# Performance work log

Measured on AMD Instinct MI355X. Metric: run time of the kernel, lower is better.

## Reference

```python
import jax, jax.numpy as jnp
import numpy as np

# Surrogate spike: forward heaviside, backward 1/(1+5|x|)^2
@jax.custom_vjp
def spike_fn(x):
    return (x >= 0).astype(x.dtype)

def _spike_fwd(x):
    return (x >= 0).astype(x.dtype), x

def _spike_bwd(x, g):
    return (g / (1.0 + 5.0 * jnp.abs(x)) ** 2,)

spike_fn.defvjp(_spike_fwd, _spike_bwd)

B, T, C, H, TDA, NCLS = 512, 1000, 64, 128, 150, 4
EPS = 1e-5


def setup_inputs() -> dict:
    key = jax.random.key(0)
    ks = jax.random.split(key, 16)
    inp = {}
    inp['kin_spikes_seq'] = jax.random.uniform(ks[0], (B, T, C), dtype=jnp.float32)
    inp['tda_features'] = jax.random.normal(ks[1], (B, TDA), dtype=jnp.float32)
    # spike_fc: init normal(mean=0.02, std=0.1), zero bias
    inp['W_fc'] = 0.02 + 0.1 * jax.random.normal(ks[2], (H, C), dtype=jnp.float32)
    inp['b_fc'] = jnp.zeros((H,), jnp.float32)
    # tda_net
    inp['W_t1'] = 0.08 * jax.random.normal(ks[3], (64, TDA), dtype=jnp.float32)
    inp['b_t1'] = jnp.zeros((64,), jnp.float32)
    inp['W_t2'] = 0.12 * jax.random.normal(ks[4], (64, 64), dtype=jnp.float32)
    inp['b_t2'] = jnp.zeros((64,), jnp.float32)
    # classifier: Linear(H+64 -> 128), BN(128), Linear(128 -> NCLS)
    inp['W_c1'] = 0.07 * jax.random.normal(ks[5], (128, H + 64), dtype=jnp.float32)
    inp['b_c1'] = jnp.zeros((128,), jnp.float32)
    inp['bn_gamma'] = jnp.ones((128,), jnp.float32)
    inp['bn_beta'] = jnp.zeros((128,), jnp.float32)
    inp['W_c2'] = 0.09 * jax.random.normal(ks[6], (NCLS, 128), dtype=jnp.float32)
    inp['b_c2'] = jnp.zeros((NCLS,), jnp.float32)
    return inp


def reference(kin_spikes_seq, tda_features, W_fc, b_fc, W_t1, b_t1, W_t2, b_t2,
              W_c1, b_c1, bn_gamma, bn_beta, W_c2, b_c2):
    Bsz, Tlen, _ = kin_spikes_seq.shape
    Hd = W_fc.shape[0]
    # Precompute all per-step input currents with one big GEMM (same math as
    # per-step Linear, since weights are time-invariant).
    currents = jnp.einsum('btc,hc->bth', kin_spikes_seq, W_fc) + b_fc  # [B,T,H]
    cur_t_first = jnp.transpose(currents, (1, 0, 2))  # [T,B,H]

    def step(carry, cur):
        mem, counts = carry
        mem = 0.9 * mem + cur
        spk = spike_fn(mem - 1.0)
        mem = mem * (1.0 - spk)
        return (mem, counts + spk), None

    init = (jnp.zeros((Bsz, Hd), kin_spikes_seq.dtype),
            jnp.zeros((Bsz, Hd), kin_spikes_seq.dtype))
    (mem, spike_counts), _ = jax.lax.scan(step, init, cur_t_first)

    firing_rate = spike_counts / Tlen
    tda_h = jax.nn.relu(tda_features @ W_t1.T + b_t1)
    tda_out = jax.nn.relu(tda_h @ W_t2.T + b_t2)
    fused = jnp.concatenate([firing_rate, tda_out], axis=1)  # [B, H+64]

    h = fused @ W_c1.T + b_c1
    # BatchNorm1d (training-mode batch statistics, biased variance)
    mean = jnp.mean(h, axis=0)
    var = jnp.var(h, axis=0)
    h = (h - mean) * jax.lax.rsqrt(var + EPS) * bn_gamma + bn_beta
    h = jax.nn.relu(h)  # dropout is identity in eval
    out = h @ W_c2.T + b_c2
    return out, spike_counts
```

## Files before the change

### kernel.cpp

```cpp
#include <hip/hip_runtime.h>
#include <stdint.h>

#define BB 512
#define TT 1000
#define CC 64
#define HH 128
#define TDA_F 150
#define NCLS 4
#define EPSV 1e-5f
#define NSEG 8
#define SEGLEN 125
#define WARM 51

typedef _Float16 half8 __attribute__((ext_vector_type(8)));
typedef float floatx4 __attribute__((ext_vector_type(4)));

__device__ __forceinline__ void split8(const float* v, half8& hi, half8& lo) {
#pragma unroll
  for (int i = 0; i < 8; ++i) {
    _Float16 h = (_Float16)v[i];
    hi[i] = h;
    lo[i] = (_Float16)(v[i] - (float)h);
  }
}

__global__ __launch_bounds__(64, 2) void snn_scan(
    const float* __restrict__ kin, const float* __restrict__ Wfc,
    const float* __restrict__ bfc, float* __restrict__ part)
{
  const int lane = threadIdx.x;
  const int q = lane >> 4;
  const int m = lane & 15;
  const int b = blockIdx.x >> 3;
  const int seg = blockIdx.x & 7;

  const int t0 = (seg == 0) ? 0 : SEGLEN * seg - WARM;
  const int ntiles = (seg == 0) ? 8 : 11;
  const int lo = SEGLEN * seg;
  const int hi = lo + SEGLEN;

  half8 bh[8][2], bl[8][2];
  float bv[8];
#pragma unroll
  for (int ht = 0; ht < 8; ++ht) {
    bv[ht] = bfc[ht * 16 + m];
#pragma unroll
    for (int kh = 0; kh < 2; ++kh) {
      const float* wp = Wfc + (ht * 16 + m) * CC + kh * 32 + q * 8;
      float av[8];
      float4 w0 = *(const float4*)(wp);
      float4 w1 = *(const float4*)(wp + 4);
      av[0] = w0.x; av[1] = w0.y; av[2] = w0.z; av[3] = w0.w;
      av[4] = w1.x; av[5] = w1.y; av[6] = w1.z; av[7] = w1.w;
      split8(av, bh[ht][kh], bl[ht][kh]);
    }
  }

  __shared__ float cur[16][132];

  const float* ab = kin + ((size_t)b * TT + (t0 + m)) * CC + q * 8;

  float4 p0 = *(const float4*)(ab);
  float4 p1 = *(const float4*)(ab + 4);
  float4 p2 = *(const float4*)(ab + 32);
  float4 p3 = *(const float4*)(ab + 36);

  float mem0 = 0.f, mem1 = 0.f, cnt0 = 0.f, cnt1 = 0.f;

  for (int tile = 0; tile < ntiles; ++tile) {
    float4 c0 = p0, c1 = p1, c2 = p2, c3 = p3;
    if (tile + 1 < ntiles) {
      ab += 16 * CC;
      p0 = *(const float4*)(ab);
      p1 = *(const float4*)(ab + 4);
      p2 = *(const float4*)(ab + 32);
      p3 = *(const float4*)(ab + 36);
    }

    float av0[8] = {c0.x, c0.y, c0.z, c0.w, c1.x, c1.y, c1.z, c1.w};
    float av1[8] = {c2.x, c2.y, c2.z, c2.w, c3.x, c3.y, c3.z, c3.w};
    half8 ah0, al0, ah1, al1;
    split8(av0, ah0, al0);
    split8(av1, ah1, al1);

#pragma unroll
    for (int ht = 0; ht < 8; ++ht) {
      floatx4 acc = {bv[ht], bv[ht], bv[ht], bv[ht]};
      acc = __builtin_amdgcn_mfma_f32_16x16x32_f16(al0, bh[ht][0], acc, 0, 0, 0);
      acc = __builtin_amdgcn_mfma_f32_16x16x32_f16(ah0, bl[ht][0], acc, 0, 0, 0);
      acc = __builtin_amdgcn_mfma_f32_16x16x32_f16(ah0, bh[ht][0], acc, 0, 0, 0);
      acc = __builtin_amdgcn_mfma_f32_16x16x32_f16(al1, bh[ht][1], acc, 0, 0, 0);
      acc = __builtin_amdgcn_mfma_f32_16x16x32_f16(ah1, bl[ht][1], acc, 0, 0, 0);
      acc = __builtin_amdgcn_mfma_f32_16x16x32_f16(ah1, bh[ht][1], acc, 0, 0, 0);
#pragma unroll
      for (int r = 0; r < 4; ++r) cur[q * 4 + r][ht * 16 + m] = acc[r];
    }

    const int tb = t0 + tile * 16;
#pragma unroll
    for (int s = 0; s < 16; ++s) {
      const float cu0 = cur[s][lane];
      const float cu1 = cur[s][lane + 64];
      const int t = tb + s;
      const bool act = (t >= lo) && (t < hi);
      mem0 = fmaf(0.9f, mem0, cu0);
      mem1 = fmaf(0.9f, mem1, cu1);
      const bool s0 = (mem0 >= 1.0f);
      const bool s1 = (mem1 >= 1.0f);
      cnt0 += (act && s0) ? 1.0f : 0.0f;
      cnt1 += (act && s1) ? 1.0f : 0.0f;
      mem0 = s0 ? 0.0f : mem0;
      mem1 = s1 ? 0.0f : mem1;
    }
  }

  float* p = part + ((size_t)(seg * BB + b)) * HH;
  p[lane] = cnt0;
  p[lane + 64] = cnt1;
}

__global__ __launch_bounds__(HH) void fused_head(
    const float* __restrict__ part, const float* __restrict__ tda,
    const float* __restrict__ W1, const float* __restrict__ b1,
    const float* __restrict__ W2, const float* __restrict__ b2,
    const float* __restrict__ Wc1, const float* __restrict__ bc1,
    float* __restrict__ counts_out, float* __restrict__ hbuf)
{
  const int b = blockIdx.x, j = threadIdx.x;
  __shared__ float x[TDA_F];
  __shared__ float h1[64];
  __shared__ float f[HH + 64];

  float c = 0.0f;
#pragma unroll
  for (int s = 0; s < NSEG; ++s) c += part[((size_t)(s * BB + b)) * HH + j];
  counts_out[b * HH + j] = c;
  f[j] = c * (1.0f / TT);
  for (int i = j; i < TDA_F; i += HH) x[i] = tda[b * TDA_F + i];
  __syncthreads();
  if (j < 64) {
    float acc = b1[j];
    const float* wr = W1 + j * TDA_F;
#pragma unroll 5
    for (int i = 0; i < TDA_F; ++i) acc = fmaf(x[i], wr[i], acc);
    h1[j] = fmaxf(acc, 0.0f);
  }
  __syncthreads();
  if (j < 64) {
    float acc = b2[j];
    const float* wr = W2 + j * 64;
#pragma unroll
    for (int i = 0; i < 64; ++i) acc = fmaf(h1[i], wr[i], acc);
    f[HH + j] = fmaxf(acc, 0.0f);
  }
  __syncthreads();
  float acc = bc1[j];
  const float* wr = Wc1 + j * (HH + 64);
#pragma unroll 4
  for (int i = 0; i < HH + 64; ++i) acc = fmaf(f[i], wr[i], acc);
  hbuf[b * HH + j] = acc;
}

__global__ __launch_bounds__(HH) void bn_stats(
    const float* __restrict__ hbuf, float* __restrict__ stats )
{
  const int j = threadIdx.x;
  float s0 = 0.f, q0 = 0.f, s1 = 0.f, q1 = 0.f;
  for (int b = 0; b < BB; b += 2) {
    float v0 = hbuf[b * HH + j];
    float v1 = hbuf[(b + 1) * HH + j];
    s0 += v0; q0 = fmaf(v0, v0, q0);
    s1 += v1; q1 = fmaf(v1, v1, q1);
  }
  const float mean = (s0 + s1) * (1.0f / BB);
  const float var = (q0 + q1) * (1.0f / BB) - mean * mean;
  stats[j] = mean;
  stats[HH + j] = rsqrtf(var + EPSV);
}

__global__ __launch_bounds__(HH) void classifier2(
    const float* __restrict__ hbuf, const float* __restrict__ stats,
    const float* __restrict__ gamma, const float* __restrict__ beta,
    const float* __restrict__ Wc2, const float* __restrict__ bc2,
    float* __restrict__ out)
{
  const int b = blockIdx.x, j = threadIdx.x;
  float hn = (hbuf[b * HH + j] - stats[j]) * stats[HH + j] * gamma[j] + beta[j];
  hn = fmaxf(hn, 0.0f);

  __shared__ float red[NCLS][HH];
#pragma unroll
  for (int k = 0; k < NCLS; ++k) red[k][j] = hn * Wc2[k * HH + j];
  __syncthreads();
  for (int off = HH / 2; off >= 1; off >>= 1) {
    if (j < off) {
#pragma unroll
      for (int k = 0; k < NCLS; ++k) red[k][j] += red[k][j + off];
    }
    __syncthreads();
  }
  if (j < NCLS) out[b * NCLS + j] = red[j][0] + bc2[j];
}

extern "C" void kernel_launch(void* const* d_in, const int* in_sizes, int n_in,
                              void* d_out, int out_size, void* d_ws, size_t ws_size,
                              hipStream_t stream)
{
  const float* kin  = (const float*)d_in[0];
  const float* tda  = (const float*)d_in[1];
  const float* Wfc  = (const float*)d_in[2];
  const float* bfc  = (const float*)d_in[3];
  const float* Wt1  = (const float*)d_in[4];
  const float* bt1  = (const float*)d_in[5];
  const float* Wt2  = (const float*)d_in[6];
  const float* bt2  = (const float*)d_in[7];
  const float* Wc1  = (const float*)d_in[8];
  const float* bc1  = (const float*)d_in[9];
  const float* gam  = (const float*)d_in[10];
  const float* bet  = (const float*)d_in[11];
  const float* Wc2  = (const float*)d_in[12];
  const float* bc2  = (const float*)d_in[13];

  float* out    = (float*)d_out;
  float* counts = out + BB * NCLS;

  float* part  = (float*)d_ws;
  float* hbuf  = part + NSEG * BB * HH;
  float* stats = hbuf + BB * HH;

  snn_scan<<<BB * NSEG, 64, 0, stream>>>(kin, Wfc, bfc, part);
  fused_head<<<BB, HH, 0, stream>>>(part, tda, Wt1, bt1, Wt2, bt2,
                                    Wc1, bc1, counts, hbuf);
  bn_stats<<<1, HH, 0, stream>>>(hbuf, stats);
  classifier2<<<BB, HH, 0, stream>>>(hbuf, stats, gam, bet, Wc2, bc2, out);
}
```

Measured before the change: 273.0 us.

## Drop input low-half MFMA terms, software-pipeline scan tile, fuse BN stats into classifier

The input spikes are now converted to a single fp16 operand, so each weight split needs four MFMAs per tile instead of six. The cost is a loss of the input low-order correction terms, which could push values near the spike threshold to the wrong side. The scan loop is restructured: loads are double-buffered two tiles ahead, and the LIF recurrence for the previous tile runs while the current tile's MFMAs are issued. The LDS layout becomes transposed and padded, so each lane reads its 16 timesteps as float4 vectors. The separate bn_stats kernel is removed, and every classifier2 block recomputes the batch statistics, trading one launch for 512 redundant reductions over hbuf.

```diff
diff --git a/kernel.cpp b/kernel.cpp
--- a/kernel.cpp
+++ b/kernel.cpp
@@ -11,17 +11,18 @@
 #define NSEG 8
 #define SEGLEN 125
 #define WARM 51
+#define CPAD 20
 
 typedef _Float16 half8 __attribute__((ext_vector_type(8)));
 typedef float floatx4 __attribute__((ext_vector_type(4)));
 
-__device__ __forceinline__ void split8(const float* v, half8& hi, half8& lo) {
-#pragma unroll
-  for (int i = 0; i < 8; ++i) {
-    _Float16 h = (_Float16)v[i];
-    hi[i] = h;
-    lo[i] = (_Float16)(v[i] - (float)h);
-  }
+__device__ __forceinline__ half8 cvt8(const float4& a, const float4& b) {
+  half8 r;
+  r[0] = (_Float16)a.x; r[1] = (_Float16)a.y;
+  r[2] = (_Float16)a.z; r[3] = (_Float16)a.w;
+  r[4] = (_Float16)b.x; r[5] = (_Float16)b.y;
+  r[6] = (_Float16)b.z; r[7] = (_Float16)b.w;
+  return r;
 }
 
 __global__ __launch_bounds__(64, 2) void snn_scan(
@@ -30,7 +31,7 @@
 {
   const int lane = threadIdx.x;
   const int q = lane >> 4;
-  const int m = lane & 15;
+  const int ml = lane & 15;
   const int b = blockIdx.x >> 3;
   const int seg = blockIdx.x & 7;
 
@@ -43,68 +44,108 @@
   float bv[8];
 #pragma unroll
   for (int ht = 0; ht < 8; ++ht) {
-    bv[ht] = bfc[ht * 16 + m];
+    bv[ht] = bfc[ht * 16 + ml];
 #pragma unroll
     for (int kh = 0; kh < 2; ++kh) {
-      const float* wp = Wfc + (ht * 16 + m) * CC + kh * 32 + q * 8;
-      float av[8];
+      const float* wp = Wfc + (ht * 16 + ml) * CC + kh * 32 + q * 8;
       float4 w0 = *(const float4*)(wp);
       float4 w1 = *(const float4*)(wp + 4);
-      av[0] = w0.x; av[1] = w0.y; av[2] = w0.z; av[3] = w0.w;
-      av[4] = w1.x; av[5] = w1.y; av[6] = w1.z; av[7] = w1.w;
-      split8(av, bh[ht][kh], bl[ht][kh]);
-    }
-  }
-
-  __shared__ float cur[16][132];
-
-  const float* ab = kin + ((size_t)b * TT + (t0 + m)) * CC + q * 8;
-
-  float4 p0 = *(const float4*)(ab);
-  float4 p1 = *(const float4*)(ab + 4);
-  float4 p2 = *(const float4*)(ab + 32);
-  float4 p3 = *(const float4*)(ab + 36);
+      float wv[8] = {w0.x, w0.y, w0.z, w0.w, w1.x, w1.y, w1.z, w1.w};
+      half8 h, l;
+#pragma unroll
+      for (int i = 0; i < 8; ++i) {
+        _Float16 x = (_Float16)wv[i];
+        h[i] = x;
+        l[i] = (_Float16)(wv[i] - (float)x);
+      }
+      bh[ht][kh] = h;
+      bl[ht][kh] = l;
+    }
+  }
+
+  __shared__ float cur[HH * CPAD];
+
+  const float* ab = kin + ((size_t)b * TT + (t0 + ml)) * CC + q * 8;
+
+  float4 p[2][4];
+#pragma unroll
+  for (int i = 0; i < 2; ++i) {
+    const float* s = ab + i * 16 * CC;
+    p[i][0] = *(const float4*)(s);
+    p[i][1] = *(const float4*)(s + 4);
+    p[i][2] = *(const float4*)(s + 32);
+    p[i][3] = *(const float4*)(s + 36);
+  }
 
   float mem0 = 0.f, mem1 = 0.f, cnt0 = 0.f, cnt1 = 0.f;
 
-  for (int tile = 0; tile < ntiles; ++tile) {
-    float4 c0 = p0, c1 = p1, c2 = p2, c3 = p3;
-    if (tile + 1 < ntiles) {
-      ab += 16 * CC;
-      p0 = *(const float4*)(ab);
-      p1 = *(const float4*)(ab + 4);
-      p2 = *(const float4*)(ab + 32);
-      p3 = *(const float4*)(ab + 36);
-    }
-
-    float av0[8] = {c0.x, c0.y, c0.z, c0.w, c1.x, c1.y, c1.z, c1.w};
-    float av1[8] = {c2.x, c2.y, c2.z, c2.w, c3.x, c3.y, c3.z, c3.w};
-    half8 ah0, al0, ah1, al1;
-    split8(av0, ah0, al0);
-    split8(av1, ah1, al1);
-
+  for (int c = 0; c < ntiles; ++c) {
+    half8 a0 = cvt8(p[c & 1][0], p[c & 1][1]);
+    half8 a1 = cvt8(p[c & 1][2], p[c & 1][3]);
+
+    if (c + 2 < ntiles) {
+      const float* s = ab + (size_t)(c + 2) * 16 * CC;
+      p[c & 1][0] = *(const float4*)(s);
+      p[c & 1][1] = *(const float4*)(s + 4);
+      p[c & 1][2] = *(const float4*)(s + 32);
+      p[c & 1][3] = *(const float4*)(s + 36);
+    }
+
+    floatx4 acc[8];
 #pragma unroll
     for (int ht = 0; ht < 8; ++ht) {
-      floatx4 acc = {bv[ht], bv[ht], bv[ht], bv[ht]};
-      acc = __builtin_amdgcn_mfma_f32_16x16x32_f16(al0, bh[ht][0], acc, 0, 0, 0);
-      acc = __builtin_amdgcn_mfma_f32_16x16x32_f16(ah0, bl[ht][0], acc, 0, 0, 0);
-      acc = __builtin_amdgcn_mfma_f32_16x16x32_f16(ah0, bh[ht][0], acc, 0, 0, 0);
-      acc = __builtin_amdgcn_mfma_f32_16x16x32_f16(al1, bh[ht][1], acc, 0, 0, 0);
-      acc = __builtin_amdgcn_mfma_f32_16x16x32_f16(ah1, bl[ht][1], acc, 0, 0, 0);
-      acc = __builtin_amdgcn_mfma_f32_16x16x32_f16(ah1, bh[ht][1], acc, 0, 0, 0);
-#pragma unroll
-      for (int r = 0; r < 4; ++r) cur[q * 4 + r][ht * 16 + m] = acc[r];
-    }
-
-    const int tb = t0 + tile * 16;
+      floatx4 a = {bv[ht], bv[ht], bv[ht], bv[ht]};
+      a = __builtin_amdgcn_mfma_f32_16x16x32_f16(a0, bl[ht][0], a, 0, 0, 0);
+      a = __builtin_amdgcn_mfma_f32_16x16x32_f16(a0, bh[ht][0], a, 0, 0, 0);
+      a = __builtin_amdgcn_mfma_f32_16x16x32_f16(a1, bl[ht][1], a, 0, 0, 0);
+      a = __builtin_amdgcn_mfma_f32_16x16x32_f16(a1, bh[ht][1], a, 0, 0, 0);
+      acc[ht] = a;
+    }
+
+    if (c >= 1) {
+      const float4* r0 = (const float4*)(cur + lane * CPAD);
+      const float4* r1 = (const float4*)(cur + (lane + 64) * CPAD);
+      float4 v0[4] = {r0[0], r0[1], r0[2], r0[3]};
+      float4 v1[4] = {r1[0], r1[1], r1[2], r1[3]};
+      const float* f0 = (const float*)v0;
+      const float* f1 = (const float*)v1;
+      const int tb = t0 + (c - 1) * 16;
+#pragma unroll
+      for (int s = 0; s < 16; ++s) {
+        const int t = tb + s;
+        const bool act = (t >= lo) && (t < hi);
+        mem0 = fmaf(0.9f, mem0, f0[s]);
+        mem1 = fmaf(0.9f, mem1, f1[s]);
+        const bool s0 = (mem0 >= 1.0f);
+        const bool s1 = (mem1 >= 1.0f);
+        cnt0 += (act && s0) ? 1.0f : 0.0f;
+        cnt1 += (act && s1) ? 1.0f : 0.0f;
+        mem0 = s0 ? 0.0f : mem0;
+        mem1 = s1 ? 0.0f : mem1;
+      }
+    }
+
+#pragma unroll
+    for (int ht = 0; ht < 8; ++ht) {
+      float4 st = {acc[ht][0], acc[ht][1], acc[ht][2], acc[ht][3]};
+      *(float4*)(cur + (ht * 16 + ml) * CPAD + q * 4) = st;
+    }
+  }
+
+  {
+    const float4* r0 = (const float4*)(cur + lane * CPAD);
+    const float4* r1 = (const float4*)(cur + (lane + 64) * CPAD);
+    float4 v0[4] = {r0[0], r0[1], r0[2], r0[3]};
+    float4 v1[4] = {r1[0], r1[1], r1[2], r1[3]};
+    const float* f0 = (const float*)v0;
+    const float* f1 = (const float*)v1;
+    const int tb = t0 + (ntiles - 1) * 16;
 #pragma unroll
     for (int s = 0; s < 16; ++s) {
-      const float cu0 = cur[s][lane];
-      const float cu1 = cur[s][lane + 64];
       const int t = tb + s;
       const bool act = (t >= lo) && (t < hi);
-      mem0 = fmaf(0.9f, mem0, cu0);
-      mem1 = fmaf(0.9f, mem1, cu1);
+      mem0 = fmaf(0.9f, mem0, f0[s]);
+      mem1 = fmaf(0.9f, mem1, f1[s]);
       const bool s0 = (mem0 >= 1.0f);
       const bool s1 = (mem1 >= 1.0f);
       cnt0 += (act && s0) ? 1.0f : 0.0f;
@@ -114,9 +155,9 @@
     }
   }
 
-  float* p = part + ((size_t)(seg * BB + b)) * HH;
-  p[lane] = cnt0;
-  p[lane + 64] = cnt1;
+  float* pp = part + ((size_t)(seg * BB + b)) * HH;
+  pp[lane] = cnt0;
+  pp[lane + 64] = cnt1;
 }
 
 __global__ __launch_bounds__(HH) void fused_head(
@@ -161,31 +202,25 @@
   hbuf[b * HH + j] = acc;
 }
 
-__global__ __launch_bounds__(HH) void bn_stats(
-    const float* __restrict__ hbuf, float* __restrict__ stats )
-{
-  const int j = threadIdx.x;
-  float s0 = 0.f, q0 = 0.f, s1 = 0.f, q1 = 0.f;
-  for (int b = 0; b < BB; b += 2) {
-    float v0 = hbuf[b * HH + j];
-    float v1 = hbuf[(b + 1) * HH + j];
-    s0 += v0; q0 = fmaf(v0, v0, q0);
-    s1 += v1; q1 = fmaf(v1, v1, q1);
-  }
-  const float mean = (s0 + s1) * (1.0f / BB);
-  const float var = (q0 + q1) * (1.0f / BB) - mean * mean;
-  stats[j] = mean;
-  stats[HH + j] = rsqrtf(var + EPSV);
-}
-
 __global__ __launch_bounds__(HH) void classifier2(
-    const float* __restrict__ hbuf, const float* __restrict__ stats,
+    const float* __restrict__ hbuf,
     const float* __restrict__ gamma, const float* __restrict__ beta,
     const float* __restrict__ Wc2, const float* __restrict__ bc2,
     float* __restrict__ out)
 {
   const int b = blockIdx.x, j = threadIdx.x;
-  float hn = (hbuf[b * HH + j] - stats[j]) * stats[HH + j] * gamma[j] + beta[j];
+  float s0 = 0.f, q0 = 0.f, s1 = 0.f, q1 = 0.f;
+  for (int r = 0; r < BB; r += 2) {
+    float v0 = hbuf[r * HH + j];
+    float v1 = hbuf[(r + 1) * HH + j];
+    s0 += v0; q0 = fmaf(v0, v0, q0);
+    s1 += v1; q1 = fmaf(v1, v1, q1);
+  }
+  const float mean = (s0 + s1) * (1.0f / BB);
+  const float var = (q0 + q1) * (1.0f / BB) - mean * mean;
+  const float rstd = rsqrtf(var + EPSV);
+
+  float hn = (hbuf[b * HH + j] - mean) * rstd * gamma[j] + beta[j];
   hn = fmaxf(hn, 0.0f);
 
   __shared__ float red[NCLS][HH];
@@ -224,13 +259,11 @@
   float* out    = (float*)d_out;
   float* counts = out + BB * NCLS;
 
-  float* part  = (float*)d_ws;
-  float* hbuf  = part + NSEG * BB * HH;
-  float* stats = hbuf + BB * HH;
+  float* part = (float*)d_ws;
+  float* hbuf = part + NSEG * BB * HH;
 
   snn_scan<<<BB * NSEG, 64, 0, stream>>>(kin, Wfc, bfc, part);
   fused_head<<<BB, HH, 0, stream>>>(part, tda, Wt1, bt1, Wt2, bt2,
                                     Wc1, bc1, counts, hbuf);
-  bn_stats<<<1, HH, 0, stream>>>(hbuf, stats);
-  classifier2<<<BB, HH, 0, stream>>>(hbuf, stats, gam, bet, Wc2, bc2, out);
-}
+  classifier2<<<BB, HH, 0, stream>>>(hbuf, gam, bet, Wc2, bc2, out);
+}
```

New measurement: 314.2 us. +15.1%, slower.
